# Kernel optimization log

Measured on AMD Instinct MI355X. Metric: run time of the kernel, lower is better.

The kernel has to match this reference:

```python
import jax, jax.numpy as jnp
import numpy as np

HEADS = 4

def _axial_attn(xs, wqkv, wproj, bproj, heads=HEADS):
    # xs: [B', C, L]; wqkv: [3C, C]; wproj: [C, C]; bproj: [C]
    Bp, C, L = xs.shape
    hd = C // heads
    scale = hd ** -0.5
    qkv = jnp.einsum('oc,bcl->bol', wqkv, xs)  # [B', 3C, L]
    q, k, v = jnp.split(qkv, 3, axis=1)
    q = q.reshape(Bp, heads, hd, L)
    k = k.reshape(Bp, heads, hd, L)
    v = v.reshape(Bp, heads, hd, L)
    attn = jax.nn.softmax(jnp.einsum('bhdi,bhdj->bhij', q, k) * scale, axis=-1)
    out = jnp.einsum('bhij,bhdj->bhdi', attn, v).reshape(Bp, C, L)
    return jnp.einsum('oc,bcl->bol', wproj, out) + bproj[None, :, None]

def setup_inputs() -> dict:
    key = jax.random.key(0)
    ks = jax.random.split(key, 7)
    B, C, H, W = 8, 128, 128, 128
    return {
        'x': jax.random.normal(ks[0], (B, C, H, W), dtype=jnp.float32),
        'wqkv_h': jax.random.normal(ks[1], (3 * C, C), dtype=jnp.float32) * 0.05,
        'wproj_h': jax.random.normal(ks[2], (C, C), dtype=jnp.float32) * 0.05,
        'bproj_h': jax.random.normal(ks[3], (C,), dtype=jnp.float32) * 0.05,
        'wqkv_w': jax.random.normal(ks[4], (3 * C, C), dtype=jnp.float32) * 0.05,
        'wproj_w': jax.random.normal(ks[5], (C, C), dtype=jnp.float32) * 0.05,
        'bproj_w': jax.random.normal(ks[6], (C,), dtype=jnp.float32) * 0.05,
    }

def reference(x, wqkv_h, wproj_h, bproj_h, wqkv_w, wproj_w, bproj_w):
    B, C, H, W = x.shape
    # height pass: rows become batch, attend along W
    xh = x.transpose(0, 2, 1, 3).reshape(B * H, C, W)
    xh = _axial_attn(xh, wqkv_h, wproj_h, bproj_h)
    xh = xh.reshape(B, H, C, W).transpose(0, 2, 1, 3)
    # width pass: cols become batch, attend along H
    xw = x.transpose(0, 3, 1, 2).reshape(B * W, C, H)
    xw = _axial_attn(xw, wqkv_w, wproj_w, bproj_w)
    xw = xw.reshape(B, W, C, H).transpose(0, 2, 3, 1)
    return (xh + xw) / 2
```

## Files before the change

### kernel.cpp

```cpp
#include <hip/hip_runtime.h>
#include <hip/hip_bf16.h>
#include <stdint.h>

typedef __attribute__((ext_vector_type(8))) short short8v;
typedef __attribute__((ext_vector_type(4))) float f32x4;
typedef unsigned short u16;
typedef unsigned int u32;

__device__ __align__(16) u16 g_xh [8u * 128u * 128u * 128u];
__device__ __align__(16) u16 g_xTw[8u * 128u * 128u * 128u];
__device__ __align__(16) u16 g_W2 [8u * 128u * 128u * 128u];
__device__ __align__(16) u16 g_wqkvP[2u * 49152u];
__device__ __align__(16) u16 g_wpP [2u * 16384u];

#define XST_OFF 0
#define QT_OFF  32768
#define KT_OFF  43008
#define VH_OFF  53248
#define OT_OFF  61952
#define SMEM_BYTES 72192

__device__ __forceinline__ u16 f2bf(float f) {
    u32 b = __float_as_uint(f);
    b += 0x7FFFu + ((b >> 16) & 1u);
    return (u16)(b >> 16);
}
__device__ __forceinline__ u32 pk2(float a, float b) {
    __hip_bfloat162 h = __float22bfloat162_rn(make_float2(a, b));
    union { __hip_bfloat162 h; u32 u; } cv; cv.h = h; return cv.u;
}
__device__ __forceinline__ float bf2f(u16 u) {
    return __uint_as_float(((u32)u) << 16);
}

__global__ __launch_bounds__(512)
void prep_weights(const float* __restrict__ wqkv_h, const float* __restrict__ wproj_h,
                  const float* __restrict__ wqkv_w, const float* __restrict__ wproj_w)
{
    const float QSC = 0.17677669529663687f;
    int id = blockIdx.x * 512 + threadIdx.x;
    if (id < 12288) {
        int p = id / 6144, i2 = id % 6144;
        int h = i2 / 1536, i3 = i2 % 1536;
        int t = i3 / 256,  i4 = i3 % 256;
        int kk = i4 / 64,  lane = i4 % 64;
        int cc = lane & 15, qq = lane >> 4;
        int r96 = t * 16 + cc;
        int g = r96 >> 5, rl = r96 & 31;
        const float* src = (p == 0 ? wqkv_h : wqkv_w) + (g * 128 + h * 32 + rl) * 128 + kk * 32 + qq * 8;
        float4 a = *(const float4*)src;
        float4 c = *(const float4*)(src + 4);
        float s = (g == 0) ? QSC : 1.0f;
        *(uint4*)(g_wqkvP + (size_t)id * 8) =
            make_uint4(pk2(a.x * s, a.y * s), pk2(a.z * s, a.w * s),
                       pk2(c.x * s, c.y * s), pk2(c.z * s, c.w * s));
    } else {
        int id2 = id - 12288;
        int p = id2 / 2048, i2 = id2 % 2048;
        int h = i2 / 512,  i3 = i2 % 512;
        int t = i3 / 64,   lane = i3 % 64;
        int cc = lane & 15, qq = lane >> 4;
        int o = t * 16 + cc;
        const float* src = (p == 0 ? wproj_h : wproj_w) + o * 128 + h * 32 + qq * 8;
        float4 a = *(const float4*)src;
        float4 c = *(const float4*)(src + 4);
        *(uint4*)(g_wpP + (size_t)id2 * 8) =
            make_uint4(pk2(a.x, a.y), pk2(a.z, a.w), pk2(c.x, c.y), pk2(c.z, c.w));
    }
}

__global__ __launch_bounds__(256)
void transpose_x(const float* __restrict__ x)
{
    __shared__ char tsm[32768];
    const int b = blockIdx.x >> 6;
    const int hp = blockIdx.x & 63;
    const int tid = threadIdx.x;
    for (int hh = 0; hh < 2; ++hh) {
        const int h = hp * 2 + hh;
        #pragma unroll
        for (int it = 0; it < 16; ++it) {
            int task = it * 256 + tid;
            int w = task & 127, c4 = task >> 7;
            const float* p = x + (size_t)b * 2097152 + (c4 * 4) * 16384 + h * 128 + w;
            u32 u0 = pk2(p[0], p[16384]);
            u32 u1 = pk2(p[2 * 16384], p[3 * 16384]);
            int off = w * 256 + ((((c4 >> 1) << 4) ^ ((w & 7) << 4)) | ((c4 & 1) << 3));
            *(uint2*)(tsm + off) = make_uint2(u0, u1);
        }
        __syncthreads();
        #pragma unroll
        for (int it = 0; it < 8; ++it) {
            int i = it * 256 + tid;
            *(uint4*)(g_xh + (size_t)(b * 128 + h) * 16384 + i * 8) = *(const uint4*)(tsm + i * 16);
        }
        #pragma unroll
        for (int it = 0; it < 8; ++it) {
            int i = it * 256 + tid;
            int w = i >> 4, c8 = i & 15;
            uint4 v = *(const uint4*)(tsm + w * 256 + ((c8 << 4) ^ ((w & 7) << 4)));
            size_t ds = ((size_t)(b * 128 + w) * 128 + h) * 128 + (((c8 << 4) ^ ((h & 7) << 4)) >> 1);
            *(uint4*)(g_xTw + ds) = v;
        }
        __syncthreads();
    }
}

__global__ __launch_bounds__(512, 4)
void attn_kernel(const float* __restrict__ bias_h, const float* __restrict__ bias_w,
                 float* __restrict__ out)
{
    extern __shared__ char smem[];
    const int t    = threadIdx.x;
    const int lane = t & 63;
    const int wv   = t >> 6;
    const int cc   = lane & 15;
    const int qq   = lane >> 4;
    const int pass = blockIdx.x >> 10;
    const int b    = (blockIdx.x >> 7) & 7;
    const int row  = blockIdx.x & 127;
    const f32x4 zf4 = (f32x4){0.f, 0.f, 0.f, 0.f};

    {
        const u16* slab = (pass ? g_xTw : g_xh) + (size_t)(b * 128 + row) * 16384;
        #pragma unroll
        for (int it = 0; it < 4; ++it) {
            int idx = t + 512 * it;
            *(uint4*)(smem + XST_OFF + idx * 16) = *(const uint4*)(slab + idx * 8);
        }
    }

    const float* bias = pass ? bias_w : bias_h;
    float biasr[4];
    #pragma unroll
    for (int r = 0; r < 4; ++r) biasr[r] = bias[wv * 16 + 4 * qq + r];

    f32x4 yacc[8];
    #pragma unroll
    for (int i = 0; i < 8; ++i) yacc[i] = zf4;

    __syncthreads();

    const int og = wv & 1;
    const int lg = wv >> 1;

    for (int h = 0; h < 4; ++h) {
        const u16* wb  = g_wqkvP + (size_t)(pass * 4 + h) * 12288;
        const u16* wpb = g_wpP   + (size_t)(pass * 4 + h) * 4096 + (wv * 64 + lane) * 8;

        {
            f32x4 acc[3][2];
            #pragma unroll
            for (int ot = 0; ot < 3; ++ot)
                #pragma unroll
                for (int lt = 0; lt < 2; ++lt) acc[ot][lt] = zf4;
            __builtin_amdgcn_s_setprio(1);
            #pragma unroll
            for (int kk = 0; kk < 4; ++kk) {
                short8v A[3], Bf[2];
                #pragma unroll
                for (int ot = 0; ot < 3; ++ot)
                    A[ot] = *(const short8v*)(wb + (((og * 3 + ot) * 4 + kk) * 64 + lane) * 8);
                #pragma unroll
                for (int lt = 0; lt < 2; ++lt) {
                    int l = lg * 32 + lt * 16 + cc;
                    Bf[lt] = *(const short8v*)(smem + XST_OFF + l * 256 + (((kk * 64 + qq * 16)) ^ ((l & 7) << 4)));
                }
                #pragma unroll
                for (int ot = 0; ot < 3; ++ot)
                    #pragma unroll
                    for (int lt = 0; lt < 2; ++lt)
                        acc[ot][lt] = __builtin_amdgcn_mfma_f32_16x16x32_bf16(A[ot], Bf[lt], acc[ot][lt], 0, 0, 0);
            }
            __builtin_amdgcn_s_setprio(0);
            #pragma unroll
            for (int ot = 0; ot < 3; ++ot) {
                int got = og * 3 + ot;
                #pragma unroll
                for (int lt = 0; lt < 2; ++lt) {
                    int l0 = (lg * 2 + lt) * 16 + cc;
                    f32x4 v = acc[ot][lt];
                    if (got < 2) {
                        *(uint2*)(smem + QT_OFF + l0 * 80 + (got * 16 + 4 * qq) * 2) =
                            make_uint2(pk2(v[0], v[1]), pk2(v[2], v[3]));
                    } else if (got < 4) {
                        *(uint2*)(smem + KT_OFF + l0 * 80 + ((got - 2) * 16 + 4 * qq) * 2) =
                            make_uint2(pk2(v[0], v[1]), pk2(v[2], v[3]));
                    } else {
                        int d0 = (got - 4) * 16 + 4 * qq;
                        #pragma unroll
                        for (int r = 0; r < 4; ++r)
                            *(u16*)(smem + VH_OFF + (d0 + r) * 272 + l0 * 2) = f2bf(v[r]);
                    }
                }
            }
        }
        __syncthreads();

        f32x4 sacc[8];
        {
            short8v aq = *(const short8v*)(smem + QT_OFF + (wv * 16 + cc) * 80 + qq * 16);
            __builtin_amdgcn_s_setprio(1);
            #pragma unroll
            for (int jt = 0; jt < 8; ++jt) {
                short8v bk = *(const short8v*)(smem + KT_OFF + (jt * 16 + cc) * 80 + qq * 16);
                sacc[jt] = __builtin_amdgcn_mfma_f32_16x16x32_bf16(bk, aq, zf4, 0, 0, 0);
            }
            __builtin_amdgcn_s_setprio(0);
        }
        float mx = -3.4e38f;
        #pragma unroll
        for (int jt = 0; jt < 8; ++jt)
            #pragma unroll
            for (int r = 0; r < 4; ++r) mx = fmaxf(mx, sacc[jt][r]);
        mx = fmaxf(mx, __shfl_xor(mx, 16));
        mx = fmaxf(mx, __shfl_xor(mx, 32));
        float sm = 0.f;
        #pragma unroll
        for (int jt = 0; jt < 8; ++jt)
            #pragma unroll
            for (int r = 0; r < 4; ++r) {
                float p = exp2f((sacc[jt][r] - mx) * 1.4426950408889634f);
                sacc[jt][r] = p;
                sm += p;
            }
        sm += __shfl_xor(sm, 16);
        sm += __shfl_xor(sm, 32);
        float rden = 1.0f / sm;
        u32 u[8][2];
        #pragma unroll
        for (int jt = 0; jt < 8; ++jt) {
            u[jt][0] = pk2(sacc[jt][0], sacc[jt][1]);
            u[jt][1] = pk2(sacc[jt][2], sacc[jt][3]);
        }

        f32x4 oacc[2] = {zf4, zf4};
        const int base = cc + ((qq & 1) << 5);
        const bool hiT = (qq >> 1) != 0;
        __builtin_amdgcn_s_setprio(1);
        #pragma unroll
        for (int kt = 0; kt < 4; ++kt) {
            int a0 = __shfl((int)u[2 * kt][0], base),      a1 = __shfl((int)u[2 * kt][1], base);
            int a2 = __shfl((int)u[2 * kt][0], base + 16), a3 = __shfl((int)u[2 * kt][1], base + 16);
            int b0 = __shfl((int)u[2 * kt + 1][0], base),      b1 = __shfl((int)u[2 * kt + 1][1], base);
            int b2 = __shfl((int)u[2 * kt + 1][0], base + 16), b3 = __shfl((int)u[2 * kt + 1][1], base + 16);
            union { uint4 u4; short8v s8; } pf;
            pf.u4 = make_uint4((u32)(hiT ? b0 : a0), (u32)(hiT ? b1 : a1),
                               (u32)(hiT ? b2 : a2), (u32)(hiT ? b3 : a3));
            #pragma unroll
            for (int dt = 0; dt < 2; ++dt) {
                short8v vf = *(const short8v*)(smem + VH_OFF + (dt * 16 + cc) * 272 + kt * 64 + qq * 16);
                oacc[dt] = __builtin_amdgcn_mfma_f32_16x16x32_bf16(vf, pf.s8, oacc[dt], 0, 0, 0);
            }
        }
        __builtin_amdgcn_s_setprio(0);
        #pragma unroll
        for (int dt = 0; dt < 2; ++dt) {
            *(uint2*)(smem + OT_OFF + (wv * 16 + cc) * 80 + (dt * 16 + 4 * qq) * 2) =
                make_uint2(pk2(oacc[dt][0] * rden, oacc[dt][1] * rden),
                           pk2(oacc[dt][2] * rden, oacc[dt][3] * rden));
        }
        __syncthreads();

        {
            short8v aw = *(const short8v*)wpb;
            __builtin_amdgcn_s_setprio(1);
            #pragma unroll
            for (int it = 0; it < 8; ++it) {
                short8v of = *(const short8v*)(smem + OT_OFF + (it * 16 + cc) * 80 + qq * 16);
                yacc[it] = __builtin_amdgcn_mfma_f32_16x16x32_bf16(aw, of, yacc[it], 0, 0, 0);
            }
            __builtin_amdgcn_s_setprio(0);
        }
    }

    #pragma unroll
    for (int it = 0; it < 8; ++it) {
        #pragma unroll
        for (int r = 0; r < 4; ++r) {
            float y = (yacc[it][r] + biasr[r]) * 0.5f;
            int o = wv * 16 + 4 * qq + r;
            int l = it * 16 + cc;
            size_t idx = ((size_t)(b * 128 + o) * 128 + row) * 128 + l;
            if (pass == 0) out[idx] = y;
            else           g_W2[idx] = f2bf(y);
        }
    }
}

__global__ __launch_bounds__(256)
void merge_w(float* __restrict__ out)
{
    __shared__ char msm[128 * 264];
    const int b = blockIdx.x >> 7;
    const int o = blockIdx.x & 127;
    const int tid = threadIdx.x;
    const u16* slab = g_W2 + (size_t)(b * 128 + o) * 16384;
    #pragma unroll
    for (int it = 0; it < 8; ++it) {
        int i = it * 256 + tid;
        int w = i >> 4, h8 = i & 15;
        *(uint4*)(msm + w * 264 + h8 * 16) = *(const uint4*)(slab + w * 128 + h8 * 8);
    }
    __syncthreads();
    float* op = out + (size_t)(b * 128 + o) * 16384;
    #pragma unroll
    for (int it = 0; it < 8; ++it) {
        int i = it * 256 + tid;
        int h = i >> 4, w8 = i & 15;
        float f[8];
        #pragma unroll
        for (int k = 0; k < 8; ++k)
            f[k] = bf2f(*(const u16*)(msm + (w8 * 8 + k) * 264 + h * 2));
        float* dp = op + h * 128 + w8 * 8;
        float4 v0 = *(float4*)dp;
        float4 v1 = *(float4*)(dp + 4);
        v0.x += f[0]; v0.y += f[1]; v0.z += f[2]; v0.w += f[3];
        v1.x += f[4]; v1.y += f[5]; v1.z += f[6]; v1.w += f[7];
        *(float4*)dp = v0;
        *(float4*)(dp + 4) = v1;
    }
}

extern "C" void kernel_launch(void* const* d_in, const int* in_sizes, int n_in,
                              void* d_out, int out_size, void* d_ws, size_t ws_size,
                              hipStream_t stream)
{
    const float* x       = (const float*)d_in[0];
    const float* wqkv_h  = (const float*)d_in[1];
    const float* wproj_h = (const float*)d_in[2];
    const float* bproj_h = (const float*)d_in[3];
    const float* wqkv_w  = (const float*)d_in[4];
    const float* wproj_w = (const float*)d_in[5];
    const float* bproj_w = (const float*)d_in[6];
    float* out = (float*)d_out;

    (void)hipFuncSetAttribute((const void*)attn_kernel,
                              hipFuncAttributeMaxDynamicSharedMemorySize, SMEM_BYTES);

    prep_weights<<<dim3(32), dim3(512), 0, stream>>>(wqkv_h, wproj_h, wqkv_w, wproj_w);
    transpose_x<<<dim3(512), dim3(256), 0, stream>>>(x);
    attn_kernel<<<dim3(2048), dim3(512), SMEM_BYTES, stream>>>(bproj_h, bproj_w, out);
    merge_w<<<dim3(1024), dim3(256), 0, stream>>>(out);
}
```

Measured before the change: 170.3 us.

## Read x directly in height pass and store height output as bf16

```diff
diff --git a/kernel.cpp b/kernel.cpp
--- a/kernel.cpp
+++ b/kernel.cpp
@@ -7,8 +7,8 @@
 typedef unsigned short u16;
 typedef unsigned int u32;
 
-__device__ __align__(16) u16 g_xh [8u * 128u * 128u * 128u];
 __device__ __align__(16) u16 g_xTw[8u * 128u * 128u * 128u];
+__device__ __align__(16) u16 g_W1 [8u * 128u * 128u * 128u];
 __device__ __align__(16) u16 g_W2 [8u * 128u * 128u * 128u];
 __device__ __align__(16) u16 g_wqkvP[2u * 49152u];
 __device__ __align__(16) u16 g_wpP [2u * 16384u];
@@ -92,11 +92,6 @@
         #pragma unroll
         for (int it = 0; it < 8; ++it) {
             int i = it * 256 + tid;
-            *(uint4*)(g_xh + (size_t)(b * 128 + h) * 16384 + i * 8) = *(const uint4*)(tsm + i * 16);
-        }
-        #pragma unroll
-        for (int it = 0; it < 8; ++it) {
-            int i = it * 256 + tid;
             int w = i >> 4, c8 = i & 15;
             uint4 v = *(const uint4*)(tsm + w * 256 + ((c8 << 4) ^ ((w & 7) << 4)));
             size_t ds = ((size_t)(b * 128 + w) * 128 + h) * 128 + (((c8 << 4) ^ ((h & 7) << 4)) >> 1);
@@ -107,8 +102,8 @@
 }
 
 __global__ __launch_bounds__(512, 4)
-void attn_kernel(const float* __restrict__ bias_h, const float* __restrict__ bias_w,
-                 float* __restrict__ out)
+void attn_kernel(const float* __restrict__ x,
+                 const float* __restrict__ bias_h, const float* __restrict__ bias_w)
 {
     extern __shared__ char smem[];
     const int t    = threadIdx.x;
@@ -121,8 +116,20 @@
     const int row  = blockIdx.x & 127;
     const f32x4 zf4 = (f32x4){0.f, 0.f, 0.f, 0.f};
 
-    {
-        const u16* slab = (pass ? g_xTw : g_xh) + (size_t)(b * 128 + row) * 16384;
+    if (pass == 0) {
+        #pragma unroll
+        for (int it = 0; it < 4; ++it) {
+            int task = t + 512 * it;
+            int l = task & 127, c8 = task >> 7;
+            const float* p = x + (size_t)b * 2097152 + (c8 * 8) * 16384 + row * 128 + l;
+            u32 u0 = pk2(p[0], p[16384]);
+            u32 u1 = pk2(p[2 * 16384], p[3 * 16384]);
+            u32 u2 = pk2(p[4 * 16384], p[5 * 16384]);
+            u32 u3 = pk2(p[6 * 16384], p[7 * 16384]);
+            *(uint4*)(smem + XST_OFF + l * 256 + ((c8 * 16) ^ ((l & 7) << 4))) = make_uint4(u0, u1, u2, u3);
+        }
+    } else {
+        const u16* slab = g_xTw + (size_t)(b * 128 + row) * 16384;
         #pragma unroll
         for (int it = 0; it < 4; ++it) {
             int idx = t + 512 * it;
@@ -274,6 +281,7 @@
         }
     }
 
+    u16* dst = pass ? g_W2 : g_W1;
     #pragma unroll
     for (int it = 0; it < 8; ++it) {
         #pragma unroll
@@ -282,8 +290,7 @@
             int o = wv * 16 + 4 * qq + r;
             int l = it * 16 + cc;
             size_t idx = ((size_t)(b * 128 + o) * 128 + row) * 128 + l;
-            if (pass == 0) out[idx] = y;
-            else           g_W2[idx] = f2bf(y);
+            dst[idx] = f2bf(y);
         }
     }
 }
@@ -303,20 +310,27 @@
         *(uint4*)(msm + w * 264 + h8 * 16) = *(const uint4*)(slab + w * 128 + h8 * 8);
     }
     __syncthreads();
+    const u16* w1p = g_W1 + (size_t)(b * 128 + o) * 16384;
     float* op = out + (size_t)(b * 128 + o) * 16384;
     #pragma unroll
     for (int it = 0; it < 8; ++it) {
         int i = it * 256 + tid;
         int h = i >> 4, w8 = i & 15;
+        uint4 w1 = *(const uint4*)(w1p + h * 128 + w8 * 8);
         float f[8];
         #pragma unroll
         for (int k = 0; k < 8; ++k)
             f[k] = bf2f(*(const u16*)(msm + (w8 * 8 + k) * 264 + h * 2));
         float* dp = op + h * 128 + w8 * 8;
-        float4 v0 = *(float4*)dp;
-        float4 v1 = *(float4*)(dp + 4);
-        v0.x += f[0]; v0.y += f[1]; v0.z += f[2]; v0.w += f[3];
-        v1.x += f[4]; v1.y += f[5]; v1.z += f[6]; v1.w += f[7];
+        float4 v0, v1;
+        v0.x = f[0] + bf2f((u16)(w1.x & 0xFFFF));
+        v0.y = f[1] + bf2f((u16)(w1.x >> 16));
+        v0.z = f[2] + bf2f((u16)(w1.y & 0xFFFF));
+        v0.w = f[3] + bf2f((u16)(w1.y >> 16));
+        v1.x = f[4] + bf2f((u16)(w1.z & 0xFFFF));
+        v1.y = f[5] + bf2f((u16)(w1.z >> 16));
+        v1.z = f[6] + bf2f((u16)(w1.w & 0xFFFF));
+        v1.w = f[7] + bf2f((u16)(w1.w >> 16));
         *(float4*)dp = v0;
         *(float4*)(dp + 4) = v1;
     }
@@ -340,6 +354,6 @@
 
     prep_weights<<<dim3(32), dim3(512), 0, stream>>>(wqkv_h, wproj_h, wqkv_w, wproj_w);
     transpose_x<<<dim3(512), dim3(256), 0, stream>>>(x);
-    attn_kernel<<<dim3(2048), dim3(512), SMEM_BYTES, stream>>>(bproj_h, bproj_w, out);
+    attn_kernel<<<dim3(2048), dim3(512), SMEM_BYTES, stream>>>(x, bproj_h, bproj_w);
     merge_w<<<dim3(1024), dim3(256), 0, stream>>>(out);
 }
```

After: 173.6 us. No clear change (+2.0%).
